# Kernel tuning notes

Measured on AMD Instinct MI355X. Metric: run time of the kernel, lower is better.

## Reference

```python
import jax, jax.numpy as jnp
import numpy as np

BATCH, SEQ, DIM = 256, 80, 1024
HEADS = 8
HID = 4 * DIM
EPS = 1e-5


def _ln(x, g, b):
    mu = jnp.mean(x, axis=-1, keepdims=True)
    var = jnp.mean((x - mu) ** 2, axis=-1, keepdims=True)
    return (x - mu) * jax.lax.rsqrt(var + EPS) * g + b


def setup_inputs() -> dict:
    key = jax.random.key(0)
    ks = jax.random.split(key, 8)
    w = lambda k, shape: jax.random.normal(k, shape, dtype=jnp.float32) * 0.02
    return {
        "x": jax.random.normal(ks[0], (BATCH, SEQ, DIM), dtype=jnp.float32),
        "Wq": w(ks[1], (DIM, DIM)),
        "Wk": w(ks[2], (DIM, DIM)),
        "Wv": w(ks[3], (DIM, DIM)),
        "bias_table": w(ks[4], (2 * SEQ - 1, HEADS)),
        "to_out_g": jnp.ones((DIM,), jnp.float32),
        "to_out_b": jnp.zeros((DIM,), jnp.float32),
        "ln1_g": jnp.ones((DIM,), jnp.float32),
        "ln1_b": jnp.zeros((DIM,), jnp.float32),
        "ln2_g": jnp.ones((DIM,), jnp.float32),
        "ln2_b": jnp.zeros((DIM,), jnp.float32),
        "fc1_w": w(ks[5], (DIM, HID)),
        "fc1_b": jnp.zeros((HID,), jnp.float32),
        "fc2_w": w(ks[6], (HID, DIM)),
        "fc2_b": jnp.zeros((DIM,), jnp.float32),
    }


def reference(x, Wq, Wk, Wv, bias_table, to_out_g, to_out_b,
              ln1_g, ln1_b, ln2_g, ln2_b, fc1_w, fc1_b, fc2_w, fc2_b):
    B, S, E = x.shape
    H = HEADS
    D = E // H
    scale = E ** (-0.5)  # NOTE: full emb_size scale, faithful to source

    q = (x @ Wq).reshape(B, S, H, D).transpose(0, 2, 1, 3)  # bhsd
    k = (x @ Wk).reshape(B, S, H, D).transpose(0, 2, 1, 3)
    v = (x @ Wv).reshape(B, S, H, D).transpose(0, 2, 1, 3)

    attn = jnp.einsum('bhqd,bhkd->bhqk', q, k) * scale
    attn = jax.nn.softmax(attn, axis=-1)

    # relative bias added AFTER softmax (non-standard, faithful)
    idx = jnp.arange(S)[:, None] - jnp.arange(S)[None, :] + (S - 1)  # [S,S] in [0,2S-2]
    bias = bias_table[idx].transpose(2, 0, 1)  # (H, S, S)
    attn = attn + bias[None]

    out = jnp.einsum('bhqk,bhkd->bhqd', attn, v)
    out = out.transpose(0, 2, 1, 3).reshape(B, S, E)
    out = _ln(out, to_out_g, to_out_b)  # LayerNorm inside attention (to_out)

    x = _ln(x + out, ln1_g, ln1_b)      # post-norm residual 1
    h = jax.nn.gelu(x @ fc1_w + fc1_b, approximate=False)  # torch nn.GELU exact
    ff = h @ fc2_w + fc2_b
    return _ln(x + ff, ln2_g, ln2_b)    # post-norm residual 2
```

## Files before the change

kernel.cpp:

```cpp
#include <hip/hip_runtime.h>
#include <stdint.h>

#define BATCH 256
#define SEQ   80
#define DIM   1024
#define HEADS 8
#define HDIM  128
#define HID   4096
#define NTOK  (BATCH * SEQ)

typedef unsigned short u16;
using short8_t = __attribute__((ext_vector_type(8))) short;
using f32x4    = __attribute__((ext_vector_type(4))) float;

__device__ __forceinline__ u16 f2bf(float f) {
  unsigned u = __float_as_uint(f);
  u += 0x7fffu + ((u >> 16) & 1u);
  return (u16)(u >> 16);
}
__device__ __forceinline__ float bf2f(u16 u) {
  return __uint_as_float(((unsigned)u) << 16);
}

__device__ __forceinline__ float gelu_exact(float v) {
  return 0.5f * v * (1.0f + erff(v * 0.70710678118654752f));
}

#define GLD16(gp, lp)                                                   \
  __builtin_amdgcn_global_load_lds(                                     \
      (__attribute__((address_space(1))) void*)(void*)(gp),             \
      (__attribute__((address_space(3))) void*)(void*)(lp), 16, 0, 0)

__global__ __launch_bounds__(256) void cast_bf16_kernel(
    const float* __restrict__ in, u16* __restrict__ out, int n4) {
  int i = blockIdx.x * 256 + threadIdx.x;
  int stride = gridDim.x * 256;
  for (; i < n4; i += stride) {
    float4 v = ((const float4*)in)[i];
    uint2 o;
    o.x = (unsigned)f2bf(v.x) | ((unsigned)f2bf(v.y) << 16);
    o.y = (unsigned)f2bf(v.z) | ((unsigned)f2bf(v.w) << 16);
    ((uint2*)out)[i] = o;
  }
}

__global__ __launch_bounds__(256) void transpose_cast_kernel(
    const float* __restrict__ in, u16* __restrict__ out, int R, int C) {
  __shared__ float tile[32][33];
  int c0 = blockIdx.x * 32, r0 = blockIdx.y * 32;
  for (int k = 0; k < 4; k++) {
    int i = threadIdx.y + k * 8;
    tile[i][threadIdx.x] = in[(size_t)(r0 + i) * C + c0 + threadIdx.x];
  }
  __syncthreads();
  for (int k = 0; k < 4; k++) {
    int i = threadIdx.y + k * 8;
    out[(size_t)(c0 + i) * R + r0 + threadIdx.x] = f2bf(tile[threadIdx.x][i]);
  }
}

template <int EPI>
__global__ __launch_bounds__(512, 2) void gemm4p(
    const u16* __restrict__ A, const u16* __restrict__ Bt,
    const float* __restrict__ bias, u16* __restrict__ outp, u16* __restrict__ outp1,
    int M, int N, int Keff, int Ks, int ntn, int ntm) {
  __shared__ __align__(16) u16 lds[65536];

  const int tid = threadIdx.x;
  const int lane = tid & 63, wave = tid >> 6;
  const int wm = wave >> 2, wn = wave & 3;
  const int lo = lane & 15, hi = lane >> 4;

  const int nwg = gridDim.x;
  int q8 = nwg >> 3, r8 = nwg & 7;
  int xcd = blockIdx.x & 7, off = blockIdx.x >> 3;
  int swz = (xcd < r8 ? xcd * (q8 + 1) : r8 * (q8 + 1) + (xcd - r8) * q8) + off;
  const int per = ntn * ntm;
  const int kp = swz / per, rem = swz % per;
  const int bn = rem % ntn, bm = rem / ntn;
  const size_t arow0 = (size_t)bm * 256, bcol0 = (size_t)bn * 256;
  const int kbase = kp * Keff;

  const int srow = tid >> 2;
  const int slb  = (tid & 3) ^ ((srow >> 1) & 3);
  const u16* sA = A + (arow0 + srow) * (size_t)Ks + kbase + slb * 8;
  const u16* sB = Bt + (bcol0 + srow) * (size_t)Ks + kbase + slb * 8;
  const size_t sstep = 128 * (size_t)Ks;

  const int arow = wm * 128 + lo;
  const int brow = wn * 64 + lo;
  const int aoff = arow * 32 + (hi ^ ((arow >> 1) & 3)) * 8;
  const int boff = brow * 32 + (hi ^ ((brow >> 1) & 3)) * 8;

  f32x4 acc[8][4] = {};
  const int NT = Keff >> 6;
  const int NI = NT >> 1;

#define STG(mat, buf, kh, t)                                                  \
  do {                                                                        \
    const u16* s_ = ((mat) ? sB : sA) + (size_t)(t) * 64 + (kh) * 32;         \
    u16* d_ = lds + ((((buf) << 2) | ((mat) << 1) | (kh)) << 13) + wave * 512;\
    GLD16(s_, d_);                                                            \
    GLD16(s_ + sstep, d_ + 4096);                                             \
  } while (0)

#define RD_A8(buf, kh, dst)                                                   \
  _Pragma("unroll") for (int mi = 0; mi < 8; ++mi)                            \
      dst[mi] = *(const short8_t*)&lds[((((buf) << 2) | (kh)) << 13) + aoff + \
                                       mi * 512];

#define RD_B4(buf, kh, dst)                                                   \
  _Pragma("unroll") for (int ni = 0; ni < 4; ++ni)                            \
      dst[ni] = *(const short8_t*)&lds[((((buf) << 2) | 2 | (kh)) << 13) +    \
                                       boff + ni * 512];

#define MFMA32(a_, b_)                                                        \
  __builtin_amdgcn_s_setprio(1);                                              \
  _Pragma("unroll") for (int mi = 0; mi < 8; ++mi)                            \
  _Pragma("unroll") for (int ni = 0; ni < 4; ++ni)                            \
      acc[mi][ni] = __builtin_amdgcn_mfma_f32_16x16x32_bf16(                  \
          a_[mi], b_[ni], acc[mi][ni], 0, 0, 0);                              \
  __builtin_amdgcn_s_setprio(0);

#define BAR()   asm volatile("s_barrier" ::: "memory")
#define LGKM0() asm volatile("s_waitcnt lgkmcnt(0)" ::: "memory")

#define PHASE(buf, kh, aR, bR, STGCODE, VMASM)                                \
  do {                                                                        \
    RD_A8(buf, kh, aR);                                                       \
    RD_B4(buf, kh, bR);                                                       \
    STGCODE;                                                                  \
    asm volatile(VMASM ::: "memory");                                         \
    BAR();                                                                    \
    LGKM0();                                                                  \
    MFMA32(aR, bR);                                                           \
  } while (0)

  STG(0, 0, 0, 0); STG(1, 0, 0, 0);
  STG(0, 0, 1, 0); STG(1, 0, 1, 0);
  STG(0, 1, 0, 1); STG(1, 1, 0, 1);
  asm volatile("s_waitcnt vmcnt(0)" ::: "memory");
  BAR();

  short8_t aX[8], bX[4], aY[8], bY[4];

  for (int i = 0; i < NI - 1; ++i) {
    const int t0 = 2 * i, t1 = 2 * i + 1;
    PHASE(0, 0, aX, bX, { STG(0, 1, 1, t1);     STG(1, 1, 1, t1); },
          "s_waitcnt vmcnt(8)");
    PHASE(0, 1, aY, bY, { STG(0, 0, 0, t0 + 2); STG(1, 0, 0, t0 + 2); },
          "s_waitcnt vmcnt(8)");
    PHASE(1, 0, aX, bX, { STG(0, 0, 1, t0 + 2); STG(1, 0, 1, t0 + 2); },
          "s_waitcnt vmcnt(8)");
    PHASE(1, 1, aY, bY, { STG(0, 1, 0, t1 + 2); STG(1, 1, 0, t1 + 2); },
          "s_waitcnt vmcnt(8)");
  }
  {
    const int t1 = NT - 1;
    PHASE(0, 0, aX, bX, { STG(0, 1, 1, t1); STG(1, 1, 1, t1); },
          "s_waitcnt vmcnt(8)");
    PHASE(0, 1, aY, bY, {}, "s_waitcnt vmcnt(4)");
    PHASE(1, 0, aX, bX, {}, "s_waitcnt vmcnt(0)");
    PHASE(1, 1, aY, bY, {}, "");
  }
#undef PHASE
#undef STG
#undef RD_A8
#undef RD_B4
#undef MFMA32

  asm volatile("s_waitcnt vmcnt(0)" ::: "memory");
  __syncthreads();

  u16* ct = lds;
#pragma unroll
  for (int n = 0; n < 4; ++n) {
    int col = wn * 64 + n * 16 + lo;
    float bv = 0.f;
    if constexpr (EPI != 0) bv = bias[bcol0 + col];
#pragma unroll
    for (int m = 0; m < 8; ++m) {
#pragma unroll
      for (int j = 0; j < 4; ++j) {
        int row = wm * 128 + m * 16 + hi * 4 + j;
        float v = acc[m][n][j] + bv;
        if constexpr (EPI == 1) v = gelu_exact(v);
        ct[row * 256 + col] = f2bf(v);
      }
    }
  }
  __syncthreads();
  u16* op = (kp ? outp1 : outp) + arow0 * (size_t)N + bcol0;
#pragma unroll
  for (int i = 0; i < 16; ++i) {
    int c = i * 512 + tid;
    int row = c >> 5, o2 = (c & 31) * 8;
    *(short8_t*)(op + (size_t)row * N + o2) = *(const short8_t*)&ct[row * 256 + o2];
  }
}

__global__ __launch_bounds__(64) void attn_kernel(
    const u16* __restrict__ QKV, const float* __restrict__ bias_table,
    u16* __restrict__ attnout) {
  __shared__ __align__(16) u16 Kt[80 * 128];
  __shared__ __align__(16) u16 Vt[96 * 128];
  __shared__ float bias_l[159];

  const int bh = blockIdx.x;
  const int b = bh >> 3, h = bh & 7;
  const int lane = threadIdx.x, lo = lane & 15, hi = lane >> 4;
  const size_t tokbase = (size_t)b * SEQ * 3072;
  const u16* Qg = QKV + tokbase + h * HDIM;
  const u16* Kg = QKV + tokbase + 1024 + h * HDIM;
  const u16* Vg = QKV + tokbase + 2048 + h * HDIM;

#pragma unroll
  for (int i = 0; i < 20; i++) {
    int flat = i * 64 + lane;
    int row = flat >> 4;
    int col = (flat & 15) * 8;
    GLD16(Kg + (size_t)row * 3072 + col, &Kt[i * 512]);
    GLD16(Vg + (size_t)row * 3072 + col, &Vt[i * 512]);
  }
  for (int i = lane; i < 16 * 128; i += 64) Vt[80 * 128 + i] = 0;
  for (int i = lane; i < 159; i += 64) bias_l[i] = bias_table[i * 8 + h];
  asm volatile("s_waitcnt vmcnt(0)" ::: "memory");
  __syncthreads();

  f32x4 sa[5][5] = {};
#pragma unroll
  for (int ks = 0; ks < 4; ks++) {
    short8_t ak[5], bq[5];
#pragma unroll
    for (int m = 0; m < 5; m++)
      ak[m] = *(const short8_t*)&Kt[(m * 16 + lo) * 128 + ks * 32 + hi * 8];
#pragma unroll
    for (int n = 0; n < 5; n++)
      bq[n] = *(const short8_t*)(Qg + (size_t)(n * 16 + lo) * 3072 + ks * 32 + hi * 8);
#pragma unroll
    for (int m = 0; m < 5; m++)
#pragma unroll
      for (int n = 0; n < 5; n++)
        sa[m][n] = __builtin_amdgcn_mfma_f32_16x16x32_bf16(ak[m], bq[n], sa[m][n], 0, 0, 0);
  }
  __syncthreads();

  u16* p_lds = Kt;
  for (int i = lane; i < 80 * 16; i += 64) {
    int q = i >> 4, c = 80 + (i & 15);
    p_lds[q * 104 + c] = 0;
  }
  const float scale = 0.03125f;
#pragma unroll
  for (int n = 0; n < 5; n++) {
    float mx = -1e30f;
#pragma unroll
    for (int m = 0; m < 5; m++)
#pragma unroll
      for (int j = 0; j < 4; j++) {
        sa[m][n][j] *= scale;
        mx = fmaxf(mx, sa[m][n][j]);
      }
    mx = fmaxf(mx, __shfl_xor(mx, 16));
    mx = fmaxf(mx, __shfl_xor(mx, 32));
    float sm = 0.f;
#pragma unroll
    for (int m = 0; m < 5; m++)
#pragma unroll
      for (int j = 0; j < 4; j++) {
        float e = __expf(sa[m][n][j] - mx);
        sa[m][n][j] = e;
        sm += e;
      }
    sm += __shfl_xor(sm, 16);
    sm += __shfl_xor(sm, 32);
    float inv = 1.0f / sm;
    int q = n * 16 + lo;
#pragma unroll
    for (int m = 0; m < 5; m++)
#pragma unroll
      for (int j = 0; j < 4; j++) {
        int key = m * 16 + hi * 4 + j;
        float pv = sa[m][n][j] * inv + bias_l[q - key + 79];
        p_lds[q * 104 + key] = f2bf(pv);
      }
  }
  __syncthreads();

#pragma unroll
  for (int half = 0; half < 2; half++) {
    f32x4 oa[5][4] = {};
#pragma unroll
    for (int ks = 0; ks < 3; ks++) {
      short8_t ap[5];
#pragma unroll
      for (int m = 0; m < 5; m++)
        ap[m] = *(const short8_t*)&p_lds[(m * 16 + lo) * 104 + ks * 32 + hi * 8];
      short8_t bv[4];
#pragma unroll
      for (int nd = 0; nd < 4; nd++) {
        int d = (half * 4 + nd) * 16 + lo;
        short8_t tt;
#pragma unroll
        for (int j = 0; j < 8; j++)
          tt[j] = (short)Vt[(ks * 32 + hi * 8 + j) * 128 + d];
        bv[nd] = tt;
      }
#pragma unroll
      for (int m = 0; m < 5; m++)
#pragma unroll
        for (int nd = 0; nd < 4; nd++)
          oa[m][nd] = __builtin_amdgcn_mfma_f32_16x16x32_bf16(ap[m], bv[nd], oa[m][nd], 0, 0, 0);
    }
#pragma unroll
    for (int m = 0; m < 5; m++)
#pragma unroll
      for (int nd = 0; nd < 4; nd++)
#pragma unroll
        for (int j = 0; j < 4; j++) {
          int q = m * 16 + hi * 4 + j;
          int d = (half * 4 + nd) * 16 + lo;
          attnout[((size_t)b * SEQ + q) * DIM + h * HDIM + d] = f2bf(oa[m][nd][j]);
        }
  }
}

__device__ __forceinline__ void block_reduce2(float& a, float& b, float* sbuf) {
#pragma unroll
  for (int m = 1; m < 64; m <<= 1) {
    a += __shfl_xor(a, m);
    b += __shfl_xor(b, m);
  }
  int w = threadIdx.x >> 6;
  if ((threadIdx.x & 63) == 0) { sbuf[w * 2] = a; sbuf[w * 2 + 1] = b; }
  __syncthreads();
  a = sbuf[0] + sbuf[2] + sbuf[4] + sbuf[6];
  b = sbuf[1] + sbuf[3] + sbuf[5] + sbuf[7];
  __syncthreads();
}

__global__ __launch_bounds__(256) void fuse1_kernel(
    const u16* __restrict__ attnout, const float* __restrict__ x,
    const float* __restrict__ og, const float* __restrict__ ob,
    const float* __restrict__ g1, const float* __restrict__ b1,
    u16* __restrict__ x1b) {
  __shared__ float sbuf[8];
  const size_t base = (size_t)blockIdx.x * DIM;
  float a[4], r[4];
  float s0 = 0.f, s1 = 0.f;
#pragma unroll
  for (int i = 0; i < 4; i++) {
    int idx = threadIdx.x + i * 256;
    a[i] = bf2f(attnout[base + idx]);
    s0 += a[i];
    s1 += a[i] * a[i];
  }
  block_reduce2(s0, s1, sbuf);
  float mu = s0 * (1.f / DIM);
  float rstd = rsqrtf(s1 * (1.f / DIM) - mu * mu + 1e-5f);
  float t0 = 0.f, t1 = 0.f;
#pragma unroll
  for (int i = 0; i < 4; i++) {
    int idx = threadIdx.x + i * 256;
    float o = (a[i] - mu) * rstd * og[idx] + ob[idx];
    r[i] = x[base + idx] + o;
    t0 += r[i];
    t1 += r[i] * r[i];
  }
  block_reduce2(t0, t1, sbuf);
  float mu2 = t0 * (1.f / DIM);
  float rstd2 = rsqrtf(t1 * (1.f / DIM) - mu2 * mu2 + 1e-5f);
#pragma unroll
  for (int i = 0; i < 4; i++) {
    int idx = threadIdx.x + i * 256;
    x1b[base + idx] = f2bf((r[i] - mu2) * rstd2 * g1[idx] + b1[idx]);
  }
}

__global__ __launch_bounds__(256) void fuse2_kernel(
    const u16* __restrict__ x1b, const u16* __restrict__ p0,
    const u16* __restrict__ p1, const float* __restrict__ fc2b,
    const float* __restrict__ g2, const float* __restrict__ b2,
    float* __restrict__ out) {
  __shared__ float sbuf[8];
  const size_t base = (size_t)blockIdx.x * DIM;
  float r[4];
  float s0 = 0.f, s1 = 0.f;
#pragma unroll
  for (int i = 0; i < 4; i++) {
    int idx = threadIdx.x + i * 256;
    r[i] = bf2f(x1b[base + idx]) + bf2f(p0[base + idx]) + bf2f(p1[base + idx]) +
           fc2b[idx];
    s0 += r[i];
    s1 += r[i] * r[i];
  }
  block_reduce2(s0, s1, sbuf);
  float mu = s0 * (1.f / DIM);
  float rstd = rsqrtf(s1 * (1.f / DIM) - mu * mu + 1e-5f);
#pragma unroll
  for (int i = 0; i < 4; i++) {
    int idx = threadIdx.x + i * 256;
    out[base + idx] = (r[i] - mu) * rstd * g2[idx] + b2[idx];
  }
}

extern "C" void kernel_launch(void* const* d_in, const int* in_sizes, int n_in,
                              void* d_out, int out_size, void* d_ws, size_t ws_size,
                              hipStream_t stream) {
  const float* x        = (const float*)d_in[0];
  const float* Wq       = (const float*)d_in[1];
  const float* Wk       = (const float*)d_in[2];
  const float* Wv       = (const float*)d_in[3];
  const float* bias_tab = (const float*)d_in[4];
  const float* og       = (const float*)d_in[5];
  const float* ob       = (const float*)d_in[6];
  const float* g1       = (const float*)d_in[7];
  const float* b1       = (const float*)d_in[8];
  const float* g2       = (const float*)d_in[9];
  const float* b2       = (const float*)d_in[10];
  const float* fc1w     = (const float*)d_in[11];
  const float* fc1b     = (const float*)d_in[12];
  const float* fc2w     = (const float*)d_in[13];
  const float* fc2b     = (const float*)d_in[14];

  char* ws = (char*)d_ws;
  u16* wqkvT = (u16*)(ws + 0);
  u16* fc1T  = (u16*)(ws + 6291456ull);
  u16* fc2T  = (u16*)(ws + 14680064ull);
  u16* pbuf  = (u16*)(ws + 23068672ull);
  u16* qbuf  = (u16*)(ws + 65011712ull);
  char* cbuf = ws + 106954752ull;
  size_t cavail = ws_size > 106954752ull ? ws_size - 106954752ull : 0;

  int cb = 1;
  while (cb < 16 && (size_t)(BATCH / cb) * SEQ * 3072 * 2 > cavail) cb <<= 1;
  int cf = 1;
  while (cf < 16 && (size_t)(NTOK / cf) * (HID + DIM) * 2 > cavail) cf <<= 1;

  dim3 tb(32, 8);
  cast_bf16_kernel<<<2048, 256, 0, stream>>>(x, qbuf, NTOK * DIM / 4);
  transpose_cast_kernel<<<dim3(32, 32), tb, 0, stream>>>(Wq, wqkvT, 1024, 1024);
  transpose_cast_kernel<<<dim3(32, 32), tb, 0, stream>>>(Wk, wqkvT + 1024 * 1024, 1024, 1024);
  transpose_cast_kernel<<<dim3(32, 32), tb, 0, stream>>>(Wv, wqkvT + 2 * 1024 * 1024, 1024, 1024);
  transpose_cast_kernel<<<dim3(128, 32), tb, 0, stream>>>(fc1w, fc1T, 1024, 4096);
  transpose_cast_kernel<<<dim3(32, 128), tb, 0, stream>>>(fc2w, fc2T, 4096, 1024);

  {
    const int nb = BATCH / cb;
    const int rows = nb * SEQ;
    u16* qkvc = (u16*)cbuf;
    const int ntm = rows / 256;
    const int nwg = ntm * 12;
    for (int c = 0; c < cb; ++c) {
      const u16* xb_c = qbuf + (size_t)c * rows * DIM;
      gemm4p<0><<<nwg, 512, 0, stream>>>(xb_c, wqkvT, nullptr, qkvc, qkvc,
                                         rows, 3072, 1024, 1024, 12, ntm);
      attn_kernel<<<nb * HEADS, 64, 0, stream>>>(
          qkvc, bias_tab, pbuf + (size_t)c * rows * DIM);
    }
  }

  fuse1_kernel<<<NTOK, 256, 0, stream>>>(pbuf, x, og, ob, g1, b1, qbuf);

  {
    const int rows = NTOK / cf;
    u16* hc  = (u16*)cbuf;
    u16* p1c = (u16*)(cbuf + (size_t)rows * HID * 2);
    const int ntm = rows / 256;
    for (int c = 0; c < cf; ++c) {
      const size_t off = (size_t)c * rows * DIM;
      gemm4p<1><<<ntm * 16, 512, 0, stream>>>(qbuf + off, fc1T, fc1b, hc, hc,
                                              rows, HID, 1024, 1024, 16, ntm);
      gemm4p<0><<<ntm * 4 * 2, 512, 0, stream>>>(hc, fc2T, nullptr,
                                                 pbuf + off, p1c,
                                                 rows, 1024, 2048, 4096, 4, ntm);
      fuse2_kernel<<<rows, 256, 0, stream>>>(qbuf + off, pbuf + off, p1c, fc2b,
                                             g2, b2, (float*)d_out + off);
    }
  }
}
```

Measured before the change: 764.3 us.

## Load GEMM B operand directly from global into registers, halve LDS

The GEMM kernel no longer stages the weight (B) tile through LDS. Each wave loads its B fragments directly from global memory into registers with inline global_load_dwordx4, double-buffered across K steps. Only A is staged in LDS, so the LDS footprint drops from 128KB to 64KB, and the epilogue writes the output in two 128-row halves to fit the smaller buffer. The aim is to cut LDS traffic and footprint, at the cost of redundant global/L2 reads of B across the wm waves, more registers, and a pipeline schedule that is harder to tune.

```diff
diff --git a/kernel.cpp b/kernel.cpp
--- a/kernel.cpp
+++ b/kernel.cpp
@@ -60,11 +60,11 @@
 }
 
 template <int EPI>
-__global__ __launch_bounds__(512, 2) void gemm4p(
+__global__ __launch_bounds__(512, 2) void gemmbd(
     const u16* __restrict__ A, const u16* __restrict__ Bt,
     const float* __restrict__ bias, u16* __restrict__ outp, u16* __restrict__ outp1,
     int M, int N, int Keff, int Ks, int ntn, int ntm) {
-  __shared__ __align__(16) u16 lds[65536];
+  __shared__ __align__(16) u16 lds[32768];
 
   const int tid = threadIdx.x;
   const int lane = tid & 63, wave = tid >> 6;
@@ -84,118 +84,130 @@
   const int srow = tid >> 2;
   const int slb  = (tid & 3) ^ ((srow >> 1) & 3);
   const u16* sA = A + (arow0 + srow) * (size_t)Ks + kbase + slb * 8;
-  const u16* sB = Bt + (bcol0 + srow) * (size_t)Ks + kbase + slb * 8;
   const size_t sstep = 128 * (size_t)Ks;
 
   const int arow = wm * 128 + lo;
-  const int brow = wn * 64 + lo;
   const int aoff = arow * 32 + (hi ^ ((arow >> 1) & 3)) * 8;
-  const int boff = brow * 32 + (hi ^ ((brow >> 1) & 3)) * 8;
+
+  const unsigned vob =
+      (unsigned)(((bcol0 + wn * 64 + lo) * (size_t)Ks + kbase + hi * 8) * 2);
 
   f32x4 acc[8][4] = {};
   const int NT = Keff >> 6;
-  const int NI = NT >> 1;
-
-#define STG(mat, buf, kh, t)                                                  \
+
+#define STG_A(par, kh, t)                                                     \
   do {                                                                        \
-    const u16* s_ = ((mat) ? sB : sA) + (size_t)(t) * 64 + (kh) * 32;         \
-    u16* d_ = lds + ((((buf) << 2) | ((mat) << 1) | (kh)) << 13) + wave * 512;\
+    const u16* s_ = sA + (size_t)(t) * 64 + (kh) * 32;                        \
+    u16* d_ = lds + ((((par) << 1) | (kh)) << 13) + wave * 512;               \
     GLD16(s_, d_);                                                            \
     GLD16(s_ + sstep, d_ + 4096);                                             \
   } while (0)
 
-#define RD_A8(buf, kh, dst)                                                   \
+#define RD_A8(par, kh, dst)                                                   \
   _Pragma("unroll") for (int mi = 0; mi < 8; ++mi)                            \
-      dst[mi] = *(const short8_t*)&lds[((((buf) << 2) | (kh)) << 13) + aoff + \
+      dst[mi] = *(const short8_t*)&lds[((((par) << 1) | (kh)) << 13) + aoff + \
                                        mi * 512];
 
-#define RD_B4(buf, kh, dst)                                                   \
-  _Pragma("unroll") for (int ni = 0; ni < 4; ++ni)                            \
-      dst[ni] = *(const short8_t*)&lds[((((buf) << 2) | 2 | (kh)) << 13) +    \
-                                       boff + ni * 512];
-
-#define MFMA32(a_, b_)                                                        \
+#define BL1(dst, n, kh, t)                                                    \
+  do {                                                                        \
+    unsigned vo_ = vob + (unsigned)(((n) * 16 * (size_t)Ks + (kh) * 32 +      \
+                                     (size_t)(t) * 64) * 2);                  \
+    asm volatile("global_load_dwordx4 %0, %1, %2"                             \
+                 : "=v"(dst) : "v"(vo_), "s"(Bt) : "memory");                 \
+  } while (0)
+
+#define BLOADALL(B_, t)                                                       \
+  do {                                                                        \
+    BL1(B_[0], 0, 0, t); BL1(B_[1], 1, 0, t);                                 \
+    BL1(B_[2], 2, 0, t); BL1(B_[3], 3, 0, t);                                 \
+    BL1(B_[4], 0, 1, t); BL1(B_[5], 1, 1, t);                                 \
+    BL1(B_[6], 2, 1, t); BL1(B_[7], 3, 1, t);                                 \
+  } while (0)
+
+#define MFMA32(a_, B_, kh)                                                    \
   __builtin_amdgcn_s_setprio(1);                                              \
   _Pragma("unroll") for (int mi = 0; mi < 8; ++mi)                            \
   _Pragma("unroll") for (int ni = 0; ni < 4; ++ni)                            \
       acc[mi][ni] = __builtin_amdgcn_mfma_f32_16x16x32_bf16(                  \
-          a_[mi], b_[ni], acc[mi][ni], 0, 0, 0);                              \
+          a_[mi], B_[(kh) * 4 + ni], acc[mi][ni], 0, 0, 0);                   \
   __builtin_amdgcn_s_setprio(0);
 
 #define BAR()   asm volatile("s_barrier" ::: "memory")
 #define LGKM0() asm volatile("s_waitcnt lgkmcnt(0)" ::: "memory")
-
-#define PHASE(buf, kh, aR, bR, STGCODE, VMASM)                                \
+#define SCHED0() __builtin_amdgcn_sched_barrier(0)
+
+#define ITER(par, t, BC, BN_, DOSTG, VMEND)                                   \
   do {                                                                        \
-    RD_A8(buf, kh, aR);                                                       \
-    RD_B4(buf, kh, bR);                                                       \
-    STGCODE;                                                                  \
-    asm volatile(VMASM ::: "memory");                                         \
+    RD_A8(par, 0, aF);                                                        \
+    asm volatile("s_waitcnt vmcnt(4)" ::: "memory"); SCHED0();                \
+    LGKM0(); MFMA32(aF, BC, 0);                                               \
+    RD_A8(par, 1, aF);                                                        \
+    BLOADALL(BN_, (t) + 1);                                                   \
+    LGKM0(); MFMA32(aF, BC, 1);                                               \
     BAR();                                                                    \
-    LGKM0();                                                                  \
-    MFMA32(aR, bR);                                                           \
+    if (DOSTG) { STG_A(par, 0, (t) + 2); STG_A(par, 1, (t) + 2); }            \
+    asm volatile(VMEND ::: "memory"); BAR();                                  \
   } while (0)
 
-  STG(0, 0, 0, 0); STG(1, 0, 0, 0);
-  STG(0, 0, 1, 0); STG(1, 0, 1, 0);
-  STG(0, 1, 0, 1); STG(1, 1, 0, 1);
+  short8_t aF[8], bX[8], bY[8];
+  STG_A(0, 0, 0); STG_A(0, 1, 0); STG_A(1, 0, 1); STG_A(1, 1, 1);
+  BLOADALL(bX, 0);
   asm volatile("s_waitcnt vmcnt(0)" ::: "memory");
   BAR();
 
-  short8_t aX[8], bX[4], aY[8], bY[4];
-
-  for (int i = 0; i < NI - 1; ++i) {
-    const int t0 = 2 * i, t1 = 2 * i + 1;
-    PHASE(0, 0, aX, bX, { STG(0, 1, 1, t1);     STG(1, 1, 1, t1); },
-          "s_waitcnt vmcnt(8)");
-    PHASE(0, 1, aY, bY, { STG(0, 0, 0, t0 + 2); STG(1, 0, 0, t0 + 2); },
-          "s_waitcnt vmcnt(8)");
-    PHASE(1, 0, aX, bX, { STG(0, 0, 1, t0 + 2); STG(1, 0, 1, t0 + 2); },
-          "s_waitcnt vmcnt(8)");
-    PHASE(1, 1, aY, bY, { STG(0, 1, 0, t1 + 2); STG(1, 1, 0, t1 + 2); },
-          "s_waitcnt vmcnt(8)");
-  }
+  for (int j = 0; j < (NT - 2) / 2; ++j) {
+    const int t0 = 2 * j;
+    ITER(0, t0,     bX, bY, 1, "s_waitcnt vmcnt(12)");
+    ITER(1, t0 + 1, bY, bX, 1, "s_waitcnt vmcnt(12)");
+  }
+  ITER(0, NT - 2, bX, bY, 0, "s_waitcnt vmcnt(8)");
   {
-    const int t1 = NT - 1;
-    PHASE(0, 0, aX, bX, { STG(0, 1, 1, t1); STG(1, 1, 1, t1); },
-          "s_waitcnt vmcnt(8)");
-    PHASE(0, 1, aY, bY, {}, "s_waitcnt vmcnt(4)");
-    PHASE(1, 0, aX, bX, {}, "s_waitcnt vmcnt(0)");
-    PHASE(1, 1, aY, bY, {}, "");
-  }
-#undef PHASE
-#undef STG
+    RD_A8(1, 0, aF);
+    asm volatile("s_waitcnt vmcnt(4)" ::: "memory"); SCHED0();
+    LGKM0(); MFMA32(aF, bY, 0);
+    RD_A8(1, 1, aF);
+    asm volatile("s_waitcnt vmcnt(0)" ::: "memory"); SCHED0();
+    LGKM0(); MFMA32(aF, bY, 1);
+  }
+#undef ITER
+#undef STG_A
 #undef RD_A8
-#undef RD_B4
+#undef BL1
+#undef BLOADALL
 #undef MFMA32
 
-  asm volatile("s_waitcnt vmcnt(0)" ::: "memory");
   __syncthreads();
 
   u16* ct = lds;
 #pragma unroll
-  for (int n = 0; n < 4; ++n) {
-    int col = wn * 64 + n * 16 + lo;
-    float bv = 0.f;
-    if constexpr (EPI != 0) bv = bias[bcol0 + col];
-#pragma unroll
-    for (int m = 0; m < 8; ++m) {
-#pragma unroll
-      for (int j = 0; j < 4; ++j) {
-        int row = wm * 128 + m * 16 + hi * 4 + j;
-        float v = acc[m][n][j] + bv;
-        if constexpr (EPI == 1) v = gelu_exact(v);
-        ct[row * 256 + col] = f2bf(v);
+  for (int half = 0; half < 2; ++half) {
+    if (wm == half) {
+#pragma unroll
+      for (int n = 0; n < 4; ++n) {
+        int col = wn * 64 + n * 16 + lo;
+        float bv = 0.f;
+        if constexpr (EPI != 0) bv = bias[bcol0 + col];
+#pragma unroll
+        for (int m = 0; m < 8; ++m) {
+#pragma unroll
+          for (int j = 0; j < 4; ++j) {
+            int row = m * 16 + hi * 4 + j;
+            float v = acc[m][n][j] + bv;
+            if constexpr (EPI == 1) v = gelu_exact(v);
+            ct[row * 256 + col] = f2bf(v);
+          }
+        }
       }
     }
-  }
-  __syncthreads();
-  u16* op = (kp ? outp1 : outp) + arow0 * (size_t)N + bcol0;
-#pragma unroll
-  for (int i = 0; i < 16; ++i) {
-    int c = i * 512 + tid;
-    int row = c >> 5, o2 = (c & 31) * 8;
-    *(short8_t*)(op + (size_t)row * N + o2) = *(const short8_t*)&ct[row * 256 + o2];
+    __syncthreads();
+    u16* op = (kp ? outp1 : outp) + (arow0 + half * 128) * (size_t)N + bcol0;
+#pragma unroll
+    for (int i = 0; i < 8; ++i) {
+      int c = i * 512 + tid;
+      int row = c >> 5, o2 = (c & 31) * 8;
+      *(short8_t*)(op + (size_t)row * N + o2) = *(const short8_t*)&ct[row * 256 + o2];
+    }
+    __syncthreads();
   }
 }
 
@@ -453,7 +465,7 @@
     const int nwg = ntm * 12;
     for (int c = 0; c < cb; ++c) {
       const u16* xb_c = qbuf + (size_t)c * rows * DIM;
-      gemm4p<0><<<nwg, 512, 0, stream>>>(xb_c, wqkvT, nullptr, qkvc, qkvc,
+      gemmbd<0><<<nwg, 512, 0, stream>>>(xb_c, wqkvT, nullptr, qkvc, qkvc,
                                          rows, 3072, 1024, 1024, 12, ntm);
       attn_kernel<<<nb * HEADS, 64, 0, stream>>>(
           qkvc, bias_tab, pbuf + (size_t)c * rows * DIM);
@@ -469,9 +481,9 @@
     const int ntm = rows / 256;
     for (int c = 0; c < cf; ++c) {
       const size_t off = (size_t)c * rows * DIM;
-      gemm4p<1><<<ntm * 16, 512, 0, stream>>>(qbuf + off, fc1T, fc1b, hc, hc,
+      gemmbd<1><<<ntm * 16, 512, 0, stream>>>(qbuf + off, fc1T, fc1b, hc, hc,
                                               rows, HID, 1024, 1024, 16, ntm);
-      gemm4p<0><<<ntm * 4 * 2, 512, 0, stream>>>(hc, fc2T, nullptr,
+      gemmbd<0><<<ntm * 4 * 2, 512, 0, stream>>>(hc, fc2T, nullptr,
                                                  pbuf + off, p1c,
                                                  rows, 1024, 2048, 4096, 4, ntm);
       fuse2_kernel<<<rows, 256, 0, stream>>>(qbuf + off, pbuf + off, p1c, fc2b,
```

New measurement: 1.006 ms. 1.32x slower.

## Replace 256x256 GEMM tile with 128x128 triple-buffered kernel

Applied to the files above, without the earlier changes.

Rewrites the GEMM kernel from a 256x256 output tile with 512 threads and a two-stage, two-half K pipeline into a 128x128 tile with 256 threads, K steps of 32, and a three-slot LDS ring buffer. LDS use drops from 128KB to 48KB and launch bounds ask for three blocks per CU. All three GEMM launches are updated to the new tile grid. Smaller tiles lower register and LDS pressure and give more blocks, but halve operand reuse per load and double global traffic per FLOP. Each K step also carries a barrier over half the MFMA work it had before.

```diff
diff --git a/kernel.cpp b/kernel.cpp
--- a/kernel.cpp
+++ b/kernel.cpp
@@ -60,15 +60,15 @@
 }
 
 template <int EPI>
-__global__ __launch_bounds__(512, 2) void gemm4p(
+__global__ __launch_bounds__(256, 3) void gemm128(
     const u16* __restrict__ A, const u16* __restrict__ Bt,
     const float* __restrict__ bias, u16* __restrict__ outp, u16* __restrict__ outp1,
     int M, int N, int Keff, int Ks, int ntn, int ntm) {
-  __shared__ __align__(16) u16 lds[65536];
+  __shared__ __align__(16) u16 lds[24576];
 
   const int tid = threadIdx.x;
   const int lane = tid & 63, wave = tid >> 6;
-  const int wm = wave >> 2, wn = wave & 3;
+  const int wm = wave >> 1, wn = wave & 1;
   const int lo = lane & 15, hi = lane >> 4;
 
   const int nwg = gridDim.x;
@@ -78,98 +78,83 @@
   const int per = ntn * ntm;
   const int kp = swz / per, rem = swz % per;
   const int bn = rem % ntn, bm = rem / ntn;
-  const size_t arow0 = (size_t)bm * 256, bcol0 = (size_t)bn * 256;
+  const size_t arow0 = (size_t)bm * 128, bcol0 = (size_t)bn * 128;
   const int kbase = kp * Keff;
 
   const int srow = tid >> 2;
   const int slb  = (tid & 3) ^ ((srow >> 1) & 3);
   const u16* sA = A + (arow0 + srow) * (size_t)Ks + kbase + slb * 8;
   const u16* sB = Bt + (bcol0 + srow) * (size_t)Ks + kbase + slb * 8;
-  const size_t sstep = 128 * (size_t)Ks;
-
-  const int arow = wm * 128 + lo;
+  const size_t sstep = 64 * (size_t)Ks;
+
+  const int arow = wm * 64 + lo;
   const int brow = wn * 64 + lo;
   const int aoff = arow * 32 + (hi ^ ((arow >> 1) & 3)) * 8;
-  const int boff = brow * 32 + (hi ^ ((brow >> 1) & 3)) * 8;
-
-  f32x4 acc[8][4] = {};
-  const int NT = Keff >> 6;
-  const int NI = NT >> 1;
-
-#define STG(mat, buf, kh, t)                                                  \
+  const int boff = 4096 + brow * 32 + (hi ^ ((brow >> 1) & 3)) * 8;
+
+  f32x4 acc[4][4] = {};
+  const int NT = Keff >> 5;
+
+#define STG(bo_, t)                                                           \
   do {                                                                        \
-    const u16* s_ = ((mat) ? sB : sA) + (size_t)(t) * 64 + (kh) * 32;         \
-    u16* d_ = lds + ((((buf) << 2) | ((mat) << 1) | (kh)) << 13) + wave * 512;\
-    GLD16(s_, d_);                                                            \
-    GLD16(s_ + sstep, d_ + 4096);                                             \
+    const u16* sa_ = sA + (size_t)(t) * 32;                                   \
+    const u16* sb_ = sB + (size_t)(t) * 32;                                   \
+    u16* da_ = lds + (bo_) * 8192 + wave * 512;                               \
+    GLD16(sa_, da_);                                                          \
+    GLD16(sa_ + sstep, da_ + 2048);                                           \
+    GLD16(sb_, da_ + 4096);                                                   \
+    GLD16(sb_ + sstep, da_ + 6144);                                           \
   } while (0)
 
-#define RD_A8(buf, kh, dst)                                                   \
-  _Pragma("unroll") for (int mi = 0; mi < 8; ++mi)                            \
-      dst[mi] = *(const short8_t*)&lds[((((buf) << 2) | (kh)) << 13) + aoff + \
-                                       mi * 512];
-
-#define RD_B4(buf, kh, dst)                                                   \
-  _Pragma("unroll") for (int ni = 0; ni < 4; ++ni)                            \
-      dst[ni] = *(const short8_t*)&lds[((((buf) << 2) | 2 | (kh)) << 13) +    \
-                                       boff + ni * 512];
-
-#define MFMA32(a_, b_)                                                        \
+#define RD(bo_, aR, bR)                                                       \
+  do {                                                                        \
+    _Pragma("unroll") for (int mi = 0; mi < 4; ++mi)                          \
+        aR[mi] = *(const short8_t*)&lds[(bo_) * 8192 + aoff + mi * 512];      \
+    _Pragma("unroll") for (int ni = 0; ni < 4; ++ni)                          \
+        bR[ni] = *(const short8_t*)&lds[(bo_) * 8192 + boff + ni * 512];      \
+  } while (0)
+
+#define MFMA16(aR, bR)                                                        \
   __builtin_amdgcn_s_setprio(1);                                              \
-  _Pragma("unroll") for (int mi = 0; mi < 8; ++mi)                            \
+  _Pragma("unroll") for (int mi = 0; mi < 4; ++mi)                            \
   _Pragma("unroll") for (int ni = 0; ni < 4; ++ni)                            \
       acc[mi][ni] = __builtin_amdgcn_mfma_f32_16x16x32_bf16(                  \
-          a_[mi], b_[ni], acc[mi][ni], 0, 0, 0);                              \
+          aR[mi], bR[ni], acc[mi][ni], 0, 0, 0);                              \
   __builtin_amdgcn_s_setprio(0);
 
 #define BAR()   asm volatile("s_barrier" ::: "memory")
 #define LGKM0() asm volatile("s_waitcnt lgkmcnt(0)" ::: "memory")
 
-#define PHASE(buf, kh, aR, bR, STGCODE, VMASM)                                \
-  do {                                                                        \
-    RD_A8(buf, kh, aR);                                                       \
-    RD_B4(buf, kh, bR);                                                       \
-    STGCODE;                                                                  \
-    asm volatile(VMASM ::: "memory");                                         \
-    BAR();                                                                    \
-    LGKM0();                                                                  \
-    MFMA32(aR, bR);                                                           \
-  } while (0)
-
-  STG(0, 0, 0, 0); STG(1, 0, 0, 0);
-  STG(0, 0, 1, 0); STG(1, 0, 1, 0);
-  STG(0, 1, 0, 1); STG(1, 1, 0, 1);
+  short8_t aR[4], bR[4];
+
+  STG(0, 0); STG(1, 1);
+  asm volatile("s_waitcnt vmcnt(4)" ::: "memory");
+  BAR();
+
+  int bo = 0, bo2 = 2;
+  for (int t = 0; t < NT - 2; ++t) {
+    RD(bo, aR, bR);
+    STG(bo2, t + 2);
+    asm volatile("s_waitcnt vmcnt(4)" ::: "memory");
+    BAR();
+    LGKM0();
+    MFMA16(aR, bR);
+    bo = (bo == 2) ? 0 : bo + 1;
+    bo2 = (bo2 == 2) ? 0 : bo2 + 1;
+  }
+  RD(bo, aR, bR);
   asm volatile("s_waitcnt vmcnt(0)" ::: "memory");
   BAR();
-
-  short8_t aX[8], bX[4], aY[8], bY[4];
-
-  for (int i = 0; i < NI - 1; ++i) {
-    const int t0 = 2 * i, t1 = 2 * i + 1;
-    PHASE(0, 0, aX, bX, { STG(0, 1, 1, t1);     STG(1, 1, 1, t1); },
-          "s_waitcnt vmcnt(8)");
-    PHASE(0, 1, aY, bY, { STG(0, 0, 0, t0 + 2); STG(1, 0, 0, t0 + 2); },
-          "s_waitcnt vmcnt(8)");
-    PHASE(1, 0, aX, bX, { STG(0, 0, 1, t0 + 2); STG(1, 0, 1, t0 + 2); },
-          "s_waitcnt vmcnt(8)");
-    PHASE(1, 1, aY, bY, { STG(0, 1, 0, t1 + 2); STG(1, 1, 0, t1 + 2); },
-          "s_waitcnt vmcnt(8)");
-  }
-  {
-    const int t1 = NT - 1;
-    PHASE(0, 0, aX, bX, { STG(0, 1, 1, t1); STG(1, 1, 1, t1); },
-          "s_waitcnt vmcnt(8)");
-    PHASE(0, 1, aY, bY, {}, "s_waitcnt vmcnt(4)");
-    PHASE(1, 0, aX, bX, {}, "s_waitcnt vmcnt(0)");
-    PHASE(1, 1, aY, bY, {}, "");
-  }
-#undef PHASE
+  LGKM0();
+  MFMA16(aR, bR);
+  bo = (bo == 2) ? 0 : bo + 1;
+  RD(bo, aR, bR);
+  LGKM0();
+  MFMA16(aR, bR);
 #undef STG
-#undef RD_A8
-#undef RD_B4
-#undef MFMA32
-
-  asm volatile("s_waitcnt vmcnt(0)" ::: "memory");
+#undef RD
+#undef MFMA16
+
   __syncthreads();
 
   u16* ct = lds;
@@ -179,23 +164,23 @@
     float bv = 0.f;
     if constexpr (EPI != 0) bv = bias[bcol0 + col];
 #pragma unroll
-    for (int m = 0; m < 8; ++m) {
+    for (int m = 0; m < 4; ++m) {
 #pragma unroll
       for (int j = 0; j < 4; ++j) {
-        int row = wm * 128 + m * 16 + hi * 4 + j;
+        int row = wm * 64 + m * 16 + hi * 4 + j;
         float v = acc[m][n][j] + bv;
         if constexpr (EPI == 1) v = gelu_exact(v);
-        ct[row * 256 + col] = f2bf(v);
+        ct[row * 128 + col] = f2bf(v);
       }
     }
   }
   __syncthreads();
   u16* op = (kp ? outp1 : outp) + arow0 * (size_t)N + bcol0;
 #pragma unroll
-  for (int i = 0; i < 16; ++i) {
-    int c = i * 512 + tid;
-    int row = c >> 5, o2 = (c & 31) * 8;
-    *(short8_t*)(op + (size_t)row * N + o2) = *(const short8_t*)&ct[row * 256 + o2];
+  for (int i = 0; i < 8; ++i) {
+    int c = i * 256 + tid;
+    int row = c >> 4, o2 = (c & 15) * 8;
+    *(short8_t*)(op + (size_t)row * N + o2) = *(const short8_t*)&ct[row * 128 + o2];
   }
 }
 
@@ -449,12 +434,12 @@
     const int nb = BATCH / cb;
     const int rows = nb * SEQ;
     u16* qkvc = (u16*)cbuf;
-    const int ntm = rows / 256;
-    const int nwg = ntm * 12;
+    const int ntm = rows / 128;
+    const int nwg = ntm * 24;
     for (int c = 0; c < cb; ++c) {
       const u16* xb_c = qbuf + (size_t)c * rows * DIM;
-      gemm4p<0><<<nwg, 512, 0, stream>>>(xb_c, wqkvT, nullptr, qkvc, qkvc,
-                                         rows, 3072, 1024, 1024, 12, ntm);
+      gemm128<0><<<nwg, 256, 0, stream>>>(xb_c, wqkvT, nullptr, qkvc, qkvc,
+                                          rows, 3072, 1024, 1024, 24, ntm);
       attn_kernel<<<nb * HEADS, 64, 0, stream>>>(
           qkvc, bias_tab, pbuf + (size_t)c * rows * DIM);
     }
@@ -466,14 +451,14 @@
     const int rows = NTOK / cf;
     u16* hc  = (u16*)cbuf;
     u16* p1c = (u16*)(cbuf + (size_t)rows * HID * 2);
-    const int ntm = rows / 256;
+    const int ntm = rows / 128;
     for (int c = 0; c < cf; ++c) {
       const size_t off = (size_t)c * rows * DIM;
-      gemm4p<1><<<ntm * 16, 512, 0, stream>>>(qbuf + off, fc1T, fc1b, hc, hc,
-                                              rows, HID, 1024, 1024, 16, ntm);
-      gemm4p<0><<<ntm * 4 * 2, 512, 0, stream>>>(hc, fc2T, nullptr,
-                                                 pbuf + off, p1c,
-                                                 rows, 1024, 2048, 4096, 4, ntm);
+      gemm128<1><<<ntm * 32, 256, 0, stream>>>(qbuf + off, fc1T, fc1b, hc, hc,
+                                               rows, HID, 1024, 1024, 32, ntm);
+      gemm128<0><<<ntm * 8 * 2, 256, 0, stream>>>(hc, fc2T, nullptr,
+                                                  pbuf + off, p1c,
+                                                  rows, 1024, 2048, 4096, 8, ntm);
       fuse2_kernel<<<rows, 256, 0, stream>>>(qbuf + off, pbuf + off, p1c, fc2b,
                                              g2, b2, (float*)d_out + off);
     }
```

After: 811.0 us. 1.06x slower.
